# Kernel optimization log

Measured on AMD Instinct MI355X. Metric: run time of the kernel, lower is better.

Reference implementation:

```python
import jax, jax.numpy as jnp
import numpy as np
import math

EPS_PHI = 1e-4
EPS_DEN = 1e-6

B, H, N, D = 4, 16, 4096, 64
M = 128  # num random features


def _phi(x, omega, is_query):
    # x: [B,H,N,D], omega: [M,D] -> [B,H,N,M]
    proj = jnp.einsum('bhnd,md->bhnm', x, omega)
    log_phi = proj - 0.5 * jnp.sum(x * x, axis=-1, keepdims=True)
    if is_query:
        log_phi = log_phi - jnp.max(log_phi, axis=-1, keepdims=True)
    else:
        log_phi = log_phi - jnp.max(log_phi)
    return jnp.exp(log_phi) / math.sqrt(omega.shape[0]) + EPS_PHI


def setup_inputs() -> dict:
    key = jax.random.key(0)
    kq, kk, kv, ko = jax.random.split(key, 4)
    return {
        'q': jax.random.normal(kq, (B, H, N, D), dtype=jnp.float32),
        'k': jax.random.normal(kk, (B, H, N, D), dtype=jnp.float32),
        'v': jax.random.normal(kv, (B, H, N, D), dtype=jnp.float32),
        'omega': jax.random.normal(ko, (M, D), dtype=jnp.float32),
    }


def reference(q, k, v, omega):
    scale = q.shape[-1] ** (-0.25)
    phi_q = _phi(q * scale, omega, is_query=True).astype(jnp.float32)
    phi_k = _phi(k * scale, omega, is_query=False).astype(jnp.float32)
    vf = v.astype(jnp.float32)

    b, h, n, m = phi_q.shape
    d = vf.shape[-1]
    # time-major for scan: [N,B,H,*]
    pq_t = jnp.moveaxis(phi_q, 2, 0)
    pk_t = jnp.moveaxis(phi_k, 2, 0)
    v_t = jnp.moveaxis(vf, 2, 0)

    S0 = jnp.zeros((b, h, m, d), jnp.float32)
    z0 = jnp.zeros((b, h, m), jnp.float32)

    def step(carry, inp):
        S, z = carry
        pq_i, pk_i, v_i = inp  # [B,H,M], [B,H,M], [B,H,D]
        S = S + jnp.einsum('bhm,bhd->bhmd', pk_i, v_i)
        z = z + pk_i
        num = jnp.einsum('bhm,bhmd->bhd', pq_i, S)
        den = jnp.sum(pq_i * z, axis=-1, keepdims=True) + EPS_DEN
        return (S, z), num / den

    _, out_t = jax.lax.scan(step, (S0, z0), (pq_t, pk_t, v_t))
    out = jnp.moveaxis(out_t, 0, 2)  # [B,H,N,D]
    return out.astype(q.dtype)
```

## Files before the change

kernel.cpp:

```cpp
#include <hip/hip_runtime.h>
#include <math.h>

#define Bq 4
#define Hq 16
#define Nq 4096
#define Dq 64
#define Mq 128
#define Cq 32
#define Lq 128
#define EPS_PHI 1e-4f
#define EPS_DEN 1e-6f
#define SCALE 0.35355339059327373f
#define INVSQRT_M 0.08838834764831845f
#define STATE_STRIDE 8320

#define KSTR 136
#define WSTR 264

#define PERM(m) (((m) & 15) * 8 + ((m) >> 4))

typedef __attribute__((ext_vector_type(8))) short bf16x8;
typedef __attribute__((ext_vector_type(4))) short s16x4;
typedef __attribute__((ext_vector_type(4))) float f32x4;

static __device__ inline f32x4 mfma16(bf16x8 a, bf16x8 b, f32x4 c) {
    return __builtin_amdgcn_mfma_f32_16x16x32_bf16(a, b, c, 0, 0, 0);
}

static __device__ inline unsigned short f2bf(float f) {
    unsigned u = __builtin_bit_cast(unsigned, f);
    u += 0x7FFF + ((u >> 16) & 1);
    return (unsigned short)(u >> 16);
}

static __device__ inline bf16x8 gfrag(const float* p, float scale) {
    float4 a = *(const float4*)p;
    float4 b = *(const float4*)(p + 4);
    union { bf16x8 v; unsigned short s[8]; } u;
    u.s[0] = f2bf(a.x * scale); u.s[1] = f2bf(a.y * scale);
    u.s[2] = f2bf(a.z * scale); u.s[3] = f2bf(a.w * scale);
    u.s[4] = f2bf(b.x * scale); u.s[5] = f2bf(b.y * scale);
    u.s[6] = f2bf(b.z * scale); u.s[7] = f2bf(b.w * scale);
    return u.v;
}

static __device__ inline bf16x8 gfrag_h(const float* p, float* hs) {
    float4 a = *(const float4*)p;
    float4 b = *(const float4*)(p + 4);
    float x0 = a.x * SCALE, x1 = a.y * SCALE, x2 = a.z * SCALE, x3 = a.w * SCALE;
    float x4 = b.x * SCALE, x5 = b.y * SCALE, x6 = b.z * SCALE, x7 = b.w * SCALE;
    *hs += x0 * x0 + x1 * x1 + x2 * x2 + x3 * x3
         + x4 * x4 + x5 * x5 + x6 * x6 + x7 * x7;
    union { bf16x8 v; unsigned short s[8]; } u;
    u.s[0] = f2bf(x0); u.s[1] = f2bf(x1); u.s[2] = f2bf(x2); u.s[3] = f2bf(x3);
    u.s[4] = f2bf(x4); u.s[5] = f2bf(x5); u.s[6] = f2bf(x6); u.s[7] = f2bf(x7);
    return u.v;
}

__global__ __launch_bounds__(512, 4) void chunkstate_kernel(
    const float* __restrict__ kin, const float* __restrict__ vin,
    const float* __restrict__ omega,
    float* __restrict__ partial, float* __restrict__ Sbuf,
    float* __restrict__ csumV) {
    __shared__ __align__(16) unsigned short PKt[128 * KSTR];
    __shared__ __align__(16) unsigned short Vt[80 * KSTR];
    __shared__ float wred[8];
    __shared__ float csum[8][64];
    const int t = threadIdx.x, w = t >> 6, lane = t & 63;
    const int c16 = lane & 15, qd = lane >> 4;
    const int bx = blockIdx.x;
    const size_t rowbase = (size_t)(bx >> 5) * Nq + (size_t)(bx & 31) * Lq;
    const float* kb = kin + rowbase * 64;
    const float* vb = vin + rowbase * 64;

    f32x4 acc[8];
    float ssum = 0.f;
    #pragma unroll
    for (int nt = 0; nt < 8; ++nt) acc[nt] = (f32x4){0.f, 0.f, 0.f, 0.f};
    #pragma unroll
    for (int kt = 0; kt < 2; ++kt) {
        bf16x8 a = gfrag_h(kb + (size_t)(16 * w + c16) * 64 + kt * 32 + qd * 8, &ssum);
        #pragma unroll
        for (int nt = 0; nt < 8; ++nt) {
            bf16x8 b = gfrag(omega + (size_t)(16 * nt + c16) * 64 + kt * 32 + qd * 8, 1.0f);
            acc[nt] = mfma16(a, b, acc[nt]);
        }
    }
    ssum += __shfl_xor(ssum, 16);
    ssum += __shfl_xor(ssum, 32);
    const float h_red = 0.5f * ssum;
    const int row0 = 16 * w + 4 * qd;
    float h4[4];
    #pragma unroll
    for (int r = 0; r < 4; ++r) h4[r] = __shfl(h_red, 4 * qd + r);

    float lmax = -1e30f;
    #pragma unroll
    for (int r = 0; r < 4; ++r) {
        #pragma unroll
        for (int nt = 0; nt < 8; ++nt) lmax = fmaxf(lmax, acc[nt][r] - h4[r]);
    }
    #pragma unroll
    for (int o = 1; o <= 32; o <<= 1) lmax = fmaxf(lmax, __shfl_xor(lmax, o));
    if (lane == 0) wred[w] = lmax;
    {
        const int d = t & 63, g = t >> 6;
        float s = 0.f;
        #pragma unroll
        for (int j = 0; j < 16; ++j) s += vb[(16 * g + j) * 64 + d];
        csum[g][d] = s;
    }
    #pragma unroll
    for (int rep = 0; rep < 8; ++rep) {
        int e2 = rep * 512 + t;
        int d = e2 & 63, l2 = e2 >> 6;
        unsigned a = f2bf(vb[(2 * l2) * 64 + d]);
        unsigned b = f2bf(vb[(2 * l2 + 1) * 64 + d]);
        *(unsigned*)&Vt[d * KSTR + 2 * l2] = a | (b << 16);
    }
    if (t < 128) Vt[64 * KSTR + t] = 0x3F80;
    __syncthreads();
    float mc = wred[0];
    #pragma unroll
    for (int i = 1; i < 8; ++i) mc = fmaxf(mc, wred[i]);
    if (t == 0) partial[bx] = mc;

    #pragma unroll
    for (int nt = 0; nt < 8; ++nt) {
        union { s16x4 v; unsigned short s[4]; } u;
        #pragma unroll
        for (int r = 0; r < 4; ++r) {
            float pk = __expf(acc[nt][r] - h4[r] - mc) * INVSQRT_M;
            u.s[r] = f2bf(pk);
        }
        *(s16x4*)&PKt[(16 * nt + c16) * KSTR + row0] = u.v;
    }
    __syncthreads();

    f32x4 acc2[5];
    #pragma unroll
    for (int nt = 0; nt < 5; ++nt) acc2[nt] = (f32x4){0.f, 0.f, 0.f, 0.f};
    #pragma unroll
    for (int kt = 0; kt < 4; ++kt) {
        bf16x8 a = *(const bf16x8*)&PKt[(16 * w + c16) * KSTR + kt * 32 + qd * 8];
        #pragma unroll
        for (int nt = 0; nt < 5; ++nt) {
            bf16x8 b = *(const bf16x8*)&Vt[(16 * nt + c16) * KSTR + kt * 32 + qd * 8];
            acc2[nt] = mfma16(a, b, acc2[nt]);
        }
    }
    float* sb = Sbuf + (size_t)bx * STATE_STRIDE;
    #pragma unroll
    for (int r = 0; r < 4; ++r) {
        #pragma unroll
        for (int nt = 0; nt < 4; ++nt)
            sb[(row0 + r) * 64 + 16 * nt + c16] = acc2[nt][r];
        if (c16 == 0) sb[8192 + row0 + r] = acc2[4][r];
    }
    if (t < 64) {
        float s = 0.f;
        #pragma unroll
        for (int g = 0; g < 8; ++g) s += csum[g][t];
        csumV[(size_t)bx * 64 + t] = s;
    }
}

__global__ void gmax_kernel(const float* __restrict__ partial, int n, float* __restrict__ gmax) {
    float m = -1e30f;
    for (int i = threadIdx.x; i < n; i += 256) m = fmaxf(m, partial[i]);
    #pragma unroll
    for (int o = 1; o <= 32; o <<= 1) m = fmaxf(m, __shfl_xor(m, o));
    __shared__ float w[4];
    if ((threadIdx.x & 63) == 0) w[threadIdx.x >> 6] = m;
    __syncthreads();
    if (threadIdx.x == 0) gmax[0] = fmaxf(fmaxf(w[0], w[1]), fmaxf(w[2], w[3]));
}

#define PBLK 33
__global__ __launch_bounds__(256) void prefix_kernel(
    float* __restrict__ Sbuf, const float* __restrict__ csumV,
    const float* __restrict__ partial, const float* __restrict__ gmaxp) {
    const int bh = blockIdx.x / PBLK;
    const int e = (blockIdx.x % PBLK) * 256 + threadIdx.x;
    if (e >= STATE_STRIDE) return;
    const float gm = gmaxp[0];
    const int isZ = (e >= 8192);
    const int d = e & 63;
    const size_t base = (size_t)bh * Cq * STATE_STRIDE + e;

    float vals[Cq];
    #pragma unroll
    for (int c = 0; c < Cq; ++c) vals[c] = Sbuf[base + (size_t)c * STATE_STRIDE];

    float running = 0.f;
    #pragma unroll
    for (int c = 0; c < Cq; ++c) {
        const int cx = bh * Cq + c;
        float sc = __expf(partial[cx] - gm);
        float ep = isZ ? (EPS_PHI * 128.0f) : (EPS_PHI * csumV[(size_t)cx * 64 + d]);
        float v = sc * vals[c] + ep;
        Sbuf[base + (size_t)c * STATE_STRIDE] = running;
        running += v;
    }
}

__global__ __launch_bounds__(512, 4) void replay_kernel(
    const float* __restrict__ q, const float* __restrict__ kin,
    const float* __restrict__ vin, const float* __restrict__ omega,
    const float* __restrict__ gmaxp, const float* __restrict__ Sbuf,
    float* __restrict__ out) {
    __shared__ __align__(16) unsigned short PK[128 * KSTR];
    __shared__ __align__(16) unsigned short Wt[80 * WSTR];
    const int t = threadIdx.x, w = t >> 6, lane = t & 63;
    const int c16 = lane & 15, qd = lane >> 4;
    const int bx = blockIdx.x;
    const size_t rowbase = (size_t)(bx >> 5) * Nq + (size_t)(bx & 31) * Lq;
    const float* qb = q + rowbase * 64;
    const float* kb = kin + rowbase * 64;
    const float* vb = vin + rowbase * 64;
    const float gmax = gmaxp[0];
    const int row0 = 16 * w + 4 * qd;
    const int arow = 16 * w + c16;

    f32x4 accq[8], acck[8];
    float ssum = 0.f;
    #pragma unroll
    for (int nt = 0; nt < 8; ++nt) {
        accq[nt] = (f32x4){0.f, 0.f, 0.f, 0.f};
        acck[nt] = (f32x4){0.f, 0.f, 0.f, 0.f};
    }
    #pragma unroll
    for (int kt = 0; kt < 2; ++kt) {
        bf16x8 aq = gfrag(qb + (size_t)arow * 64 + kt * 32 + qd * 8, SCALE);
        bf16x8 ak = gfrag_h(kb + (size_t)arow * 64 + kt * 32 + qd * 8, &ssum);
        #pragma unroll
        for (int nt = 0; nt < 8; ++nt) {
            bf16x8 b = gfrag(omega + (size_t)(16 * nt + c16) * 64 + kt * 32 + qd * 8, 1.0f);
            accq[nt] = mfma16(aq, b, accq[nt]);
            acck[nt] = mfma16(ak, b, acck[nt]);
        }
    }
    ssum += __shfl_xor(ssum, 16);
    ssum += __shfl_xor(ssum, 32);
    const float h_red = 0.5f * ssum;

    unsigned pqu[4][4];
    #pragma unroll
    for (int r = 0; r < 4; ++r) {
        float mx = accq[0][r];
        #pragma unroll
        for (int nt = 1; nt < 8; ++nt) mx = fmaxf(mx, accq[nt][r]);
        mx = fmaxf(mx, __shfl_xor(mx, 1));
        mx = fmaxf(mx, __shfl_xor(mx, 2));
        mx = fmaxf(mx, __shfl_xor(mx, 4));
        mx = fmaxf(mx, __shfl_xor(mx, 8));
        #pragma unroll
        for (int i = 0; i < 4; ++i) {
            float lo = __expf(accq[2 * i][r]     - mx) * INVSQRT_M + EPS_PHI;
            float hi = __expf(accq[2 * i + 1][r] - mx) * INVSQRT_M + EPS_PHI;
            pqu[r][i] = (unsigned)f2bf(lo) | ((unsigned)f2bf(hi) << 16);
        }
    }
    bf16x8 bq[4];
    {
        const int rsel = c16 & 3;
        #pragma unroll
        for (int kt = 0; kt < 4; ++kt) {
            const int src = 4 * kt + qd + ((c16 >> 2) << 4);
            union { bf16x8 v; unsigned u[4]; } tt;
            #pragma unroll
            for (int i = 0; i < 4; ++i) {
                unsigned v0 = __shfl(pqu[0][i], src);
                unsigned v1 = __shfl(pqu[1][i], src);
                unsigned v2 = __shfl(pqu[2][i], src);
                unsigned v3 = __shfl(pqu[3][i], src);
                unsigned s01 = (rsel & 1) ? v1 : v0;
                unsigned s23 = (rsel & 1) ? v3 : v2;
                tt.u[i] = (rsel & 2) ? s23 : s01;
            }
            bq[kt] = tt.v;
        }
    }
    #pragma unroll
    for (int r = 0; r < 4; ++r) {
        float h = __shfl(h_red, 4 * qd + r);
        union { bf16x8 v; unsigned short s[8]; } u;
        #pragma unroll
        for (int nt = 0; nt < 8; ++nt)
            u.s[nt] = f2bf(__expf(acck[nt][r] - h - gmax) * INVSQRT_M + EPS_PHI);
        *(bf16x8*)&PK[(row0 + r) * KSTR + c16 * 8] = u.v;
    }
    const float* sb = Sbuf + (size_t)bx * STATE_STRIDE;
    #pragma unroll
    for (int rep = 0; rep < 8; ++rep) {
        int e2 = rep * 512 + t;
        int d = e2 & 63, l2 = e2 >> 6;
        unsigned a = f2bf(vb[(2 * l2) * 64 + d]);
        unsigned b = f2bf(vb[(2 * l2 + 1) * 64 + d]);
        *(unsigned*)&Wt[d * WSTR + 2 * l2] = a | (b << 16);
    }
    #pragma unroll
    for (int rep = 0; rep < 16; ++rep) {
        int e = rep * 512 + t;
        int m = e >> 6, d = e & 63;
        Wt[d * WSTR + 128 + PERM(m)] = f2bf(sb[e]);
    }
    if (t < 128)      Wt[64 * WSTR + t] = 0x3F80;
    else if (t < 256) Wt[64 * WSTR + 128 + PERM(t - 128)] = f2bf(sb[8192 + (t - 128)]);
    __syncthreads();

    f32x4 a1[8];
    #pragma unroll
    for (int lt = 0; lt < 8; ++lt) {
        a1[lt] = (f32x4){0.f, 0.f, 0.f, 0.f};
        #pragma unroll
        for (int kt = 0; kt < 4; ++kt) {
            bf16x8 a = *(const bf16x8*)&PK[(16 * lt + c16) * KSTR + kt * 32 + qd * 8];
            a1[lt] = mfma16(a, bq[kt], a1[lt]);
        }
    }
    unsigned asu[8][2];
    #pragma unroll
    for (int lt = 0; lt < 8; ++lt) {
        const int lbase = 16 * lt + 4 * qd;
        float m0 = (lbase + 0 <= arow) ? a1[lt][0] : 0.f;
        float m1 = (lbase + 1 <= arow) ? a1[lt][1] : 0.f;
        float m2 = (lbase + 2 <= arow) ? a1[lt][2] : 0.f;
        float m3 = (lbase + 3 <= arow) ? a1[lt][3] : 0.f;
        asu[lt][0] = (unsigned)f2bf(m0) | ((unsigned)f2bf(m1) << 16);
        asu[lt][1] = (unsigned)f2bf(m2) | ((unsigned)f2bf(m3) << 16);
    }
    f32x4 acc2[5];
    #pragma unroll
    for (int nt = 0; nt < 5; ++nt) acc2[nt] = (f32x4){0.f, 0.f, 0.f, 0.f};
    {
        const int src0 = c16 + ((2 * qd) & 3) * 16;
        const int src1 = c16 + ((2 * qd + 1) & 3) * 16;
        const int hsel = qd >> 1;
        #pragma unroll
        for (int kt = 0; kt < 4; ++kt) {
            union { bf16x8 v; unsigned u[4]; } af;
            unsigned a00 = __shfl(asu[2 * kt][0], src0), a10 = __shfl(asu[2 * kt + 1][0], src0);
            unsigned a01 = __shfl(asu[2 * kt][1], src0), a11 = __shfl(asu[2 * kt + 1][1], src0);
            af.u[0] = hsel ? a10 : a00;
            af.u[1] = hsel ? a11 : a01;
            unsigned b00 = __shfl(asu[2 * kt][0], src1), b10 = __shfl(asu[2 * kt + 1][0], src1);
            unsigned b01 = __shfl(asu[2 * kt][1], src1), b11 = __shfl(asu[2 * kt + 1][1], src1);
            af.u[2] = hsel ? b10 : b00;
            af.u[3] = hsel ? b11 : b01;
            #pragma unroll
            for (int nt = 0; nt < 5; ++nt) {
                bf16x8 b = *(const bf16x8*)&Wt[(16 * nt + c16) * WSTR + kt * 32 + qd * 8];
                acc2[nt] = mfma16(af.v, b, acc2[nt]);
            }
        }
        #pragma unroll
        for (int kt = 4; kt < 8; ++kt) {
            #pragma unroll
            for (int nt = 0; nt < 5; ++nt) {
                bf16x8 b = *(const bf16x8*)&Wt[(16 * nt + c16) * WSTR + kt * 32 + qd * 8];
                acc2[nt] = mfma16(bq[kt - 4], b, acc2[nt]);
            }
        }
    }
    #pragma unroll
    for (int r = 0; r < 4; ++r) {
        float den = __shfl(acc2[4][r], lane & 48) + EPS_DEN;
        float rd = 1.0f / den;
        #pragma unroll
        for (int nt = 0; nt < 4; ++nt)
            out[(rowbase + row0 + r) * 64 + 16 * nt + c16] = acc2[nt][r] * rd;
    }
}

extern "C" void kernel_launch(void* const* d_in, const int* in_sizes, int n_in,
                              void* d_out, int out_size, void* d_ws, size_t ws_size,
                              hipStream_t stream) {
    const float* q     = (const float*)d_in[0];
    const float* k     = (const float*)d_in[1];
    const float* v     = (const float*)d_in[2];
    const float* omega = (const float*)d_in[3];
    float* out = (float*)d_out;
    float* ws  = (float*)d_ws;

    const int nChunks = Bq * Hq * Cq;
    float* partial = ws;
    float* gmax    = partial + nChunks;
    float* Sbuf    = gmax + 16;
    float* csumV   = Sbuf + (size_t)nChunks * STATE_STRIDE;

    chunkstate_kernel<<<nChunks, 512, 0, stream>>>(k, v, omega, partial, Sbuf, csumV);
    gmax_kernel<<<1, 256, 0, stream>>>(partial, nChunks, gmax);
    prefix_kernel<<<64 * PBLK, 256, 0, stream>>>(Sbuf, csumV, partial, gmax);
    replay_kernel<<<nChunks, 512, 0, stream>>>(q, k, v, omega, gmax, Sbuf, out);
}
```

Baseline: 360.8 us.

## Precompute bf16 transposed V, omega and state in global memory, drop LDS staging

Adds kernels that convert V into a transposed bf16 layout (also computing the chunk column sums) and omega into bf16 once. The chunk-state and replay kernels now read MFMA fragments straight from these global buffers instead of converting and transposing into LDS. The prefix kernel writes the prefix states directly as permuted bf16, and the z/denominator columns are produced by an MFMA against a ones fragment. This removes repeated fp32 loads and conversions plus LDS traffic, and the smaller LDS footprint allows a higher occupancy bound. In exchange it adds two launches, extra workspace, and uncoalesced strided global fragment loads.

```diff
diff --git a/kernel.cpp b/kernel.cpp
--- a/kernel.cpp
+++ b/kernel.cpp
@@ -15,7 +15,6 @@
 #define STATE_STRIDE 8320
 
 #define KSTR 136
-#define WSTR 264
 
 #define PERM(m) (((m) & 15) * 8 + ((m) >> 4))
 
@@ -57,21 +56,76 @@
     return u.v;
 }
 
-__global__ __launch_bounds__(512, 4) void chunkstate_kernel(
-    const float* __restrict__ kin, const float* __restrict__ vin,
-    const float* __restrict__ omega,
-    float* __restrict__ partial, float* __restrict__ Sbuf,
+static __device__ inline bf16x8 ones_frag() {
+    union { bf16x8 v; unsigned short s[8]; } u;
+    #pragma unroll
+    for (int i = 0; i < 8; ++i) u.s[i] = 0x3F80;
+    return u.v;
+}
+
+__global__ __launch_bounds__(256) void vconv_kernel(
+    const float* __restrict__ vin, unsigned short* __restrict__ vT,
     float* __restrict__ csumV) {
+    __shared__ __align__(16) unsigned short vt_lds[64 * KSTR];
+    __shared__ float csum[4][64];
+    const int t = threadIdx.x;
+    const int bx = blockIdx.x;
+    const int bh = bx >> 5;
+    const int l0 = (bx & 31) * Lq;
+    const float* vb = vin + ((size_t)bh * Nq + l0) * 64;
+    const int d = t & 63, g = t >> 6;
+
+    float s = 0.f;
+    #pragma unroll
+    for (int rep = 0; rep < 32; ++rep) {
+        int l = rep * 4 + g;
+        float x = vb[(size_t)l * 64 + d];
+        s += x;
+        vt_lds[d * KSTR + l] = f2bf(x);
+    }
+    csum[g][d] = s;
+    __syncthreads();
+    if (t < 64)
+        csumV[(size_t)bx * 64 + t] = csum[0][t] + csum[1][t] + csum[2][t] + csum[3][t];
+    unsigned short* vTb = vT + (size_t)bh * 64 * Nq + l0;
+    #pragma unroll
+    for (int rep = 0; rep < 4; ++rep) {
+        int idx = rep * 256 + t;
+        int dd = idx >> 4, seg = idx & 15;
+        *(bf16x8*)&vTb[(size_t)dd * Nq + seg * 8] =
+            *(const bf16x8*)&vt_lds[dd * KSTR + seg * 8];
+    }
+}
+
+__global__ __launch_bounds__(256) void oconv_kernel(
+    const float* __restrict__ omega, unsigned short* __restrict__ omb) {
+    const int t = threadIdx.x;
+    #pragma unroll
+    for (int rep = 0; rep < 4; ++rep) {
+        int g8 = rep * 256 + t;
+        const float* p = omega + (size_t)g8 * 8;
+        float4 a = *(const float4*)p;
+        float4 b = *(const float4*)(p + 4);
+        union { bf16x8 v; unsigned short s[8]; } u;
+        u.s[0] = f2bf(a.x); u.s[1] = f2bf(a.y); u.s[2] = f2bf(a.z); u.s[3] = f2bf(a.w);
+        u.s[4] = f2bf(b.x); u.s[5] = f2bf(b.y); u.s[6] = f2bf(b.z); u.s[7] = f2bf(b.w);
+        *(bf16x8*)&omb[(size_t)g8 * 8] = u.v;
+    }
+}
+
+__global__ __launch_bounds__(512, 8) void chunkstate_kernel(
+    const float* __restrict__ kin, const unsigned short* __restrict__ omb,
+    const unsigned short* __restrict__ vT,
+    float* __restrict__ partial, float* __restrict__ Sbuf) {
     __shared__ __align__(16) unsigned short PKt[128 * KSTR];
-    __shared__ __align__(16) unsigned short Vt[80 * KSTR];
     __shared__ float wred[8];
-    __shared__ float csum[8][64];
     const int t = threadIdx.x, w = t >> 6, lane = t & 63;
     const int c16 = lane & 15, qd = lane >> 4;
     const int bx = blockIdx.x;
-    const size_t rowbase = (size_t)(bx >> 5) * Nq + (size_t)(bx & 31) * Lq;
+    const int bh = bx >> 5;
+    const int l0 = (bx & 31) * Lq;
+    const size_t rowbase = (size_t)bh * Nq + l0;
     const float* kb = kin + rowbase * 64;
-    const float* vb = vin + rowbase * 64;
 
     f32x4 acc[8];
     float ssum = 0.f;
@@ -82,7 +136,7 @@
         bf16x8 a = gfrag_h(kb + (size_t)(16 * w + c16) * 64 + kt * 32 + qd * 8, &ssum);
         #pragma unroll
         for (int nt = 0; nt < 8; ++nt) {
-            bf16x8 b = gfrag(omega + (size_t)(16 * nt + c16) * 64 + kt * 32 + qd * 8, 1.0f);
+            bf16x8 b = *(const bf16x8*)&omb[(size_t)(16 * nt + c16) * 64 + kt * 32 + qd * 8];
             acc[nt] = mfma16(a, b, acc[nt]);
         }
     }
@@ -103,22 +157,6 @@
     #pragma unroll
     for (int o = 1; o <= 32; o <<= 1) lmax = fmaxf(lmax, __shfl_xor(lmax, o));
     if (lane == 0) wred[w] = lmax;
-    {
-        const int d = t & 63, g = t >> 6;
-        float s = 0.f;
-        #pragma unroll
-        for (int j = 0; j < 16; ++j) s += vb[(16 * g + j) * 64 + d];
-        csum[g][d] = s;
-    }
-    #pragma unroll
-    for (int rep = 0; rep < 8; ++rep) {
-        int e2 = rep * 512 + t;
-        int d = e2 & 63, l2 = e2 >> 6;
-        unsigned a = f2bf(vb[(2 * l2) * 64 + d]);
-        unsigned b = f2bf(vb[(2 * l2 + 1) * 64 + d]);
-        *(unsigned*)&Vt[d * KSTR + 2 * l2] = a | (b << 16);
-    }
-    if (t < 128) Vt[64 * KSTR + t] = 0x3F80;
     __syncthreads();
     float mc = wred[0];
     #pragma unroll
@@ -137,32 +175,30 @@
     }
     __syncthreads();
 
-    f32x4 acc2[5];
-    #pragma unroll
-    for (int nt = 0; nt < 5; ++nt) acc2[nt] = (f32x4){0.f, 0.f, 0.f, 0.f};
+    const unsigned short* vTb = vT + (size_t)bh * 64 * Nq + l0;
+    f32x4 accS[4], accz;
+    #pragma unroll
+    for (int dt = 0; dt < 4; ++dt) accS[dt] = (f32x4){0.f, 0.f, 0.f, 0.f};
+    accz = (f32x4){0.f, 0.f, 0.f, 0.f};
+    const bf16x8 ones = ones_frag();
     #pragma unroll
     for (int kt = 0; kt < 4; ++kt) {
-        bf16x8 a = *(const bf16x8*)&PKt[(16 * w + c16) * KSTR + kt * 32 + qd * 8];
-        #pragma unroll
-        for (int nt = 0; nt < 5; ++nt) {
-            bf16x8 b = *(const bf16x8*)&Vt[(16 * nt + c16) * KSTR + kt * 32 + qd * 8];
-            acc2[nt] = mfma16(a, b, acc2[nt]);
-        }
+        bf16x8 bfr = *(const bf16x8*)&PKt[(16 * w + c16) * KSTR + kt * 32 + qd * 8];
+        #pragma unroll
+        for (int dt = 0; dt < 4; ++dt) {
+            bf16x8 afr = *(const bf16x8*)&vTb[(size_t)(16 * dt + c16) * Nq + kt * 32 + qd * 8];
+            accS[dt] = mfma16(afr, bfr, accS[dt]);
+        }
+        accz = mfma16(ones, bfr, accz);
     }
     float* sb = Sbuf + (size_t)bx * STATE_STRIDE;
     #pragma unroll
-    for (int r = 0; r < 4; ++r) {
-        #pragma unroll
-        for (int nt = 0; nt < 4; ++nt)
-            sb[(row0 + r) * 64 + 16 * nt + c16] = acc2[nt][r];
-        if (c16 == 0) sb[8192 + row0 + r] = acc2[4][r];
-    }
-    if (t < 64) {
-        float s = 0.f;
-        #pragma unroll
-        for (int g = 0; g < 8; ++g) s += csum[g][t];
-        csumV[(size_t)bx * 64 + t] = s;
-    }
+    for (int dt = 0; dt < 4; ++dt) {
+        #pragma unroll
+        for (int r = 0; r < 4; ++r)
+            sb[(16 * dt + 4 * qd + r) * 128 + 16 * w + c16] = accS[dt][r];
+    }
+    if (qd == 0) sb[64 * 128 + 16 * w + c16] = accz[0];
 }
 
 __global__ void gmax_kernel(const float* __restrict__ partial, int n, float* __restrict__ gmax) {
@@ -178,14 +214,15 @@
 
 #define PBLK 33
 __global__ __launch_bounds__(256) void prefix_kernel(
-    float* __restrict__ Sbuf, const float* __restrict__ csumV,
+    const float* __restrict__ Sbuf, unsigned short* __restrict__ WtG,
+    const float* __restrict__ csumV,
     const float* __restrict__ partial, const float* __restrict__ gmaxp) {
     const int bh = blockIdx.x / PBLK;
     const int e = (blockIdx.x % PBLK) * 256 + threadIdx.x;
     if (e >= STATE_STRIDE) return;
     const float gm = gmaxp[0];
-    const int isZ = (e >= 8192);
-    const int d = e & 63;
+    const int dz = e >> 7, m = e & 127;
+    const int wcol = dz * 128 + PERM(m);
     const size_t base = (size_t)bh * Cq * STATE_STRIDE + e;
 
     float vals[Cq];
@@ -197,27 +234,27 @@
     for (int c = 0; c < Cq; ++c) {
         const int cx = bh * Cq + c;
         float sc = __expf(partial[cx] - gm);
-        float ep = isZ ? (EPS_PHI * 128.0f) : (EPS_PHI * csumV[(size_t)cx * 64 + d]);
-        float v = sc * vals[c] + ep;
-        Sbuf[base + (size_t)c * STATE_STRIDE] = running;
-        running += v;
-    }
-}
-
-__global__ __launch_bounds__(512, 4) void replay_kernel(
+        float ep = (dz == 64) ? (EPS_PHI * 128.0f)
+                              : (EPS_PHI * csumV[(size_t)cx * 64 + dz]);
+        WtG[(size_t)cx * STATE_STRIDE + wcol] = f2bf(running);
+        running += sc * vals[c] + ep;
+    }
+}
+
+__global__ __launch_bounds__(512, 8) void replay_kernel(
     const float* __restrict__ q, const float* __restrict__ kin,
-    const float* __restrict__ vin, const float* __restrict__ omega,
-    const float* __restrict__ gmaxp, const float* __restrict__ Sbuf,
-    float* __restrict__ out) {
+    const unsigned short* __restrict__ omb, const unsigned short* __restrict__ vT,
+    const unsigned short* __restrict__ WtG,
+    const float* __restrict__ gmaxp, float* __restrict__ out) {
     __shared__ __align__(16) unsigned short PK[128 * KSTR];
-    __shared__ __align__(16) unsigned short Wt[80 * WSTR];
     const int t = threadIdx.x, w = t >> 6, lane = t & 63;
     const int c16 = lane & 15, qd = lane >> 4;
     const int bx = blockIdx.x;
-    const size_t rowbase = (size_t)(bx >> 5) * Nq + (size_t)(bx & 31) * Lq;
+    const int bh = bx >> 5;
+    const int l0 = (bx & 31) * Lq;
+    const size_t rowbase = (size_t)bh * Nq + l0;
     const float* qb = q + rowbase * 64;
     const float* kb = kin + rowbase * 64;
-    const float* vb = vin + rowbase * 64;
     const float gmax = gmaxp[0];
     const int row0 = 16 * w + 4 * qd;
     const int arow = 16 * w + c16;
@@ -235,7 +272,7 @@
         bf16x8 ak = gfrag_h(kb + (size_t)arow * 64 + kt * 32 + qd * 8, &ssum);
         #pragma unroll
         for (int nt = 0; nt < 8; ++nt) {
-            bf16x8 b = gfrag(omega + (size_t)(16 * nt + c16) * 64 + kt * 32 + qd * 8, 1.0f);
+            bf16x8 b = *(const bf16x8*)&omb[(size_t)(16 * nt + c16) * 64 + kt * 32 + qd * 8];
             accq[nt] = mfma16(aq, b, accq[nt]);
             acck[nt] = mfma16(ak, b, acck[nt]);
         }
@@ -290,23 +327,6 @@
             u.s[nt] = f2bf(__expf(acck[nt][r] - h - gmax) * INVSQRT_M + EPS_PHI);
         *(bf16x8*)&PK[(row0 + r) * KSTR + c16 * 8] = u.v;
     }
-    const float* sb = Sbuf + (size_t)bx * STATE_STRIDE;
-    #pragma unroll
-    for (int rep = 0; rep < 8; ++rep) {
-        int e2 = rep * 512 + t;
-        int d = e2 & 63, l2 = e2 >> 6;
-        unsigned a = f2bf(vb[(2 * l2) * 64 + d]);
-        unsigned b = f2bf(vb[(2 * l2 + 1) * 64 + d]);
-        *(unsigned*)&Wt[d * WSTR + 2 * l2] = a | (b << 16);
-    }
-    #pragma unroll
-    for (int rep = 0; rep < 16; ++rep) {
-        int e = rep * 512 + t;
-        int m = e >> 6, d = e & 63;
-        Wt[d * WSTR + 128 + PERM(m)] = f2bf(sb[e]);
-    }
-    if (t < 128)      Wt[64 * WSTR + t] = 0x3F80;
-    else if (t < 256) Wt[64 * WSTR + 128 + PERM(t - 128)] = f2bf(sb[8192 + (t - 128)]);
     __syncthreads();
 
     f32x4 a1[8];
@@ -330,6 +350,9 @@
         asu[lt][0] = (unsigned)f2bf(m0) | ((unsigned)f2bf(m1) << 16);
         asu[lt][1] = (unsigned)f2bf(m2) | ((unsigned)f2bf(m3) << 16);
     }
+    const unsigned short* vTb = vT + (size_t)bh * 64 * Nq + l0;
+    const unsigned short* wg  = WtG + (size_t)bx * STATE_STRIDE;
+    const bf16x8 ones = ones_frag();
     f32x4 acc2[5];
     #pragma unroll
     for (int nt = 0; nt < 5; ++nt) acc2[nt] = (f32x4){0.f, 0.f, 0.f, 0.f};
@@ -349,23 +372,26 @@
             af.u[2] = hsel ? b10 : b00;
             af.u[3] = hsel ? b11 : b01;
             #pragma unroll
-            for (int nt = 0; nt < 5; ++nt) {
-                bf16x8 b = *(const bf16x8*)&Wt[(16 * nt + c16) * WSTR + kt * 32 + qd * 8];
+            for (int nt = 0; nt < 4; ++nt) {
+                bf16x8 b = *(const bf16x8*)&vTb[(size_t)(16 * nt + c16) * Nq + kt * 32 + qd * 8];
                 acc2[nt] = mfma16(af.v, b, acc2[nt]);
             }
-        }
-        #pragma unroll
-        for (int kt = 4; kt < 8; ++kt) {
+            acc2[4] = mfma16(af.v, ones, acc2[4]);
+        }
+        #pragma unroll
+        for (int kt = 0; kt < 4; ++kt) {
             #pragma unroll
-            for (int nt = 0; nt < 5; ++nt) {
-                bf16x8 b = *(const bf16x8*)&Wt[(16 * nt + c16) * WSTR + kt * 32 + qd * 8];
-                acc2[nt] = mfma16(bq[kt - 4], b, acc2[nt]);
+            for (int nt = 0; nt < 4; ++nt) {
+                bf16x8 b = *(const bf16x8*)&wg[(16 * nt + c16) * 128 + kt * 32 + qd * 8];
+                acc2[nt] = mfma16(bq[kt], b, acc2[nt]);
             }
+            bf16x8 bz = *(const bf16x8*)&wg[64 * 128 + kt * 32 + qd * 8];
+            acc2[4] = mfma16(bq[kt], bz, acc2[4]);
         }
     }
     #pragma unroll
     for (int r = 0; r < 4; ++r) {
-        float den = __shfl(acc2[4][r], lane & 48) + EPS_DEN;
+        float den = acc2[4][r] + EPS_DEN;
         float rd = 1.0f / den;
         #pragma unroll
         for (int nt = 0; nt < 4; ++nt)
@@ -386,11 +412,16 @@
     const int nChunks = Bq * Hq * Cq;
     float* partial = ws;
     float* gmax    = partial + nChunks;
-    float* Sbuf    = gmax + 16;
-    float* csumV   = Sbuf + (size_t)nChunks * STATE_STRIDE;
-
-    chunkstate_kernel<<<nChunks, 512, 0, stream>>>(k, v, omega, partial, Sbuf, csumV);
+    float* csumV   = gmax + 16;
+    unsigned short* omb = (unsigned short*)(csumV + (size_t)nChunks * 64);
+    unsigned short* vT  = omb + 8192;
+    unsigned short* WtG = vT + (size_t)64 * 64 * Nq;
+    float* Sbuf = (float*)(WtG + (size_t)nChunks * STATE_STRIDE);
+
+    vconv_kernel<<<nChunks, 256, 0, stream>>>(v, vT, csumV);
+    oconv_kernel<<<1, 256, 0, stream>>>(omega, omb);
+    chunkstate_kernel<<<nChunks, 512, 0, stream>>>(k, omb, vT, partial, Sbuf);
     gmax_kernel<<<1, 256, 0, stream>>>(partial, nChunks, gmax);
-    prefix_kernel<<<64 * PBLK, 256, 0, stream>>>(Sbuf, csumV, partial, gmax);
-    replay_kernel<<<nChunks, 512, 0, stream>>>(q, k, v, omega, gmax, Sbuf, out);
-}
+    prefix_kernel<<<64 * PBLK, 256, 0, stream>>>(Sbuf, WtG, csumV, partial, gmax);
+    replay_kernel<<<nChunks, 512, 0, stream>>>(q, k, omb, vT, WtG, gmax, out);
+}
```

New measurement: 534.8 us. +48.2%, slower.
